# Optimization experiments

Hardware: AMD Instinct MI355X
Metric: run time of the kernel (lower is better)

## Reference

```python
import jax, jax.numpy as jnp
import numpy as np

D_MODEL = 1024
N_HEADS = 16
HEAD_DIM = D_MODEL // N_HEADS
SEQ_LEN = 2048
LN_EPS = 1e-5


def setup_inputs() -> dict:
    key = jax.random.key(0)
    ks = jax.random.split(key, 7)
    s = 1.0 / np.sqrt(D_MODEL)
    h = jax.random.normal(ks[0], (SEQ_LEN, D_MODEL), dtype=jnp.float32)
    # torch nn.Linear weights are (out_features, in_features)
    W_qkv = jax.random.uniform(ks[1], (3 * D_MODEL, D_MODEL), jnp.float32, -s, s)
    b_qkv = jax.random.uniform(ks[2], (3 * D_MODEL,), jnp.float32, -s, s)
    W_out = jax.random.uniform(ks[3], (D_MODEL, D_MODEL), jnp.float32, -s, s)
    b_out = jax.random.uniform(ks[4], (D_MODEL,), jnp.float32, -s, s)
    gamma = jnp.ones((D_MODEL,), jnp.float32)
    beta = jnp.zeros((D_MODEL,), jnp.float32)
    return {"h": h, "W_qkv": W_qkv, "b_qkv": b_qkv, "W_out": W_out,
            "b_out": b_out, "gamma": gamma, "beta": beta}


def reference(h, W_qkv, b_qkv, W_out, b_out, gamma, beta):
    S = h.shape[0]
    # QKV projection: (S, 3*D)
    qkv = h @ W_qkv.T + b_qkv
    q, k, v = jnp.split(qkv, 3, axis=-1)
    # (S, D) -> (H, S, Dh)
    q = q.reshape(S, N_HEADS, HEAD_DIM).transpose(1, 0, 2)
    k = k.reshape(S, N_HEADS, HEAD_DIM).transpose(1, 0, 2)
    v = v.reshape(S, N_HEADS, HEAD_DIM).transpose(1, 0, 2)
    # scaled dot-product attention, non-causal (matches F.sdpa defaults)
    scale = 1.0 / jnp.sqrt(jnp.asarray(HEAD_DIM, dtype=h.dtype))
    scores = jnp.einsum('hqd,hkd->hqk', q, k) * scale  # (H, S, S)
    attn = jax.nn.softmax(scores, axis=-1)
    attn_out = jnp.einsum('hqk,hkd->hqd', attn, v)     # (H, S, Dh)
    attn_out = attn_out.transpose(1, 0, 2).reshape(S, D_MODEL)
    # output projection + residual + LayerNorm
    attn_out = attn_out @ W_out.T + b_out
    x = h + attn_out
    mu = jnp.mean(x, axis=-1, keepdims=True)
    var = jnp.var(x, axis=-1, keepdims=True)
    x_norm = (x - mu) * jax.lax.rsqrt(var + LN_EPS)
    return x_norm * gamma + beta
```

## Files before the change

### kernel.cpp

```cpp
#include <hip/hip_runtime.h>
#include <stdint.h>

#define SEQ 2048
#define DM 1024
#define NH 16
#define DH 64
#define LN_EPS 1e-5f

typedef __bf16 bf16x8 __attribute__((ext_vector_type(8)));
typedef float f32x4 __attribute__((ext_vector_type(4)));
typedef unsigned short u16;
typedef unsigned short u16x8 __attribute__((ext_vector_type(8)));
typedef unsigned int u32;
typedef short s16x4 __attribute__((ext_vector_type(4)));

__device__ __forceinline__ u16 f2bf(float f) {
  unsigned int u = __float_as_uint(f);
  unsigned int r = (u + 0x7fffu + ((u >> 16) & 1u)) >> 16;
  return (u16)r;
}

__device__ __forceinline__ float bf2f(u16 x) {
  return __uint_as_float(((u32)x) << 16);
}

__device__ __forceinline__ u32 packbf(float a, float b) {
  union { __bf16 h[2]; u32 u; } pw;
  pw.h[0] = (__bf16)a; pw.h[1] = (__bf16)b;
  return pw.u;
}

__device__ __forceinline__ f32x4 mfma16x16x16bf(s16x4 a, s16x4 b, f32x4 c) {
#if __has_builtin(__builtin_amdgcn_mfma_f32_16x16x16bf16_1k)
  return __builtin_amdgcn_mfma_f32_16x16x16bf16_1k(a, b, c, 0, 0, 0);
#else
  asm("v_mfma_f32_16x16x16_bf16 %0, %1, %2, %0" : "+v"(c) : "v"(a), "v"(b));
  return c;
#endif
}

#define GLD_LDS16(gp, lp) __builtin_amdgcn_global_load_lds( \
  (const __attribute__((address_space(1))) void*)(gp),      \
  (__attribute__((address_space(3))) void*)(lp), 16, 0, 0)

__global__ __launch_bounds__(256)
void k_f2bf3(const float* __restrict__ a, u16* __restrict__ oa, int na,
             const float* __restrict__ b, u16* __restrict__ ob, int nb,
             const float* __restrict__ c, u16* __restrict__ oc, int nc) {
  int i = blockIdx.x * 256 + threadIdx.x;
  const float* src;
  u16* dst;
  if (i < na) { src = a; dst = oa; }
  else if (i < na + nb) { src = b; dst = ob; i -= na; }
  else if (i < na + nb + nc) { src = c; dst = oc; i -= na + nb; }
  else return;
  float4 v = reinterpret_cast<const float4*>(src)[i];
  ushort4 o;
  o.x = f2bf(v.x); o.y = f2bf(v.y); o.z = f2bf(v.z); o.w = f2bf(v.w);
  reinterpret_cast<ushort4*>(dst)[i] = o;
}

template <int EPI, int BM, int BN, int XCDW>
__global__ __launch_bounds__(256)
void k_gemm_bt(const u16* __restrict__ A, const u16* __restrict__ B,
               const float* __restrict__ bias,
               u16* __restrict__ outb, u16* __restrict__ outv,
               int M, int N, int K) {
  constexpr int MF = BM / 32, NF = BN / 32;
  constexpr int WM = BM / 2, WN = BN / 2;
  constexpr int AG = BM / 64, BG = BN / 64;
  __shared__ u16 Alds[2][BM][32];
  __shared__ u16 Blds[2][BN][32];
  const int tid = threadIdx.x;
  const int w = tid >> 6, l = tid & 63, lg = l >> 4, lr = l & 15;
  const int wr = w >> 1, wc = w & 1;

  int bx = blockIdx.x, by = blockIdx.y, bz = blockIdx.z;
  if (XCDW > 0) {
    const int nx = gridDim.x, ny = gridDim.y;
    const int u = bx + nx * (by + ny * bz);
    const int xcd = u & 7, g = u >> 3;
    bx = xcd * XCDW + (g % XCDW);
    const int rem = g / XCDW;
    by = rem % ny;
    bz = rem / ny;
  }

  const int m0 = by * BM, n0 = bx * BN;
  const int KTall = K >> 5;
  const int ktn = KTall / gridDim.z;
  const int kt0 = bz * ktn;

  f32x4 acc[MF][NF] = {};

  auto stage = [&](int buf, int kt) {
    const int k0 = kt << 5;
    const int row = l >> 2, col = (l & 3) * 8;
#pragma unroll
    for (int p = 0; p < AG; ++p) {
      const int rbase = (w * AG + p) * 16;
      GLD_LDS16(A + (size_t)(m0 + rbase + row) * K + k0 + col, &Alds[buf][rbase][0]);
    }
#pragma unroll
    for (int p = 0; p < BG; ++p) {
      const int rbase = (w * BG + p) * 16;
      GLD_LDS16(B + (size_t)(n0 + rbase + row) * K + k0 + col, &Blds[buf][rbase][0]);
    }
  };

  auto compute = [&](int buf) {
    bf16x8 af[MF], bfr[NF];
#pragma unroll
    for (int mi = 0; mi < MF; ++mi)
      af[mi] = *reinterpret_cast<const bf16x8*>(&Alds[buf][wr * WM + mi * 16 + lr][lg * 8]);
#pragma unroll
    for (int ni = 0; ni < NF; ++ni)
      bfr[ni] = *reinterpret_cast<const bf16x8*>(&Blds[buf][wc * WN + ni * 16 + lr][lg * 8]);
#pragma unroll
    for (int mi = 0; mi < MF; ++mi)
#pragma unroll
      for (int ni = 0; ni < NF; ++ni)
        acc[mi][ni] = __builtin_amdgcn_mfma_f32_16x16x32_bf16(af[mi], bfr[ni], acc[mi][ni], 0, 0, 0);
  };

  stage(0, kt0);
  __syncthreads();
  for (int i = 0; i < ktn; ++i) {
    const int cur = i & 1;
    if (i + 1 < ktn) stage(cur ^ 1, kt0 + i + 1);
    compute(cur);
    __syncthreads();
  }

  if (EPI == 3) {
    u16* op = outb + (size_t)bz * M * N;
#pragma unroll
    for (int ni = 0; ni < NF; ++ni) {
      const int n = n0 + wc * WN + ni * 16 + lr;
#pragma unroll
      for (int mi = 0; mi < MF; ++mi) {
#pragma unroll
        for (int r = 0; r < 4; ++r) {
          const int m = m0 + wr * WM + mi * 16 + lg * 4 + r;
          op[(size_t)m * N + n] = f2bf(acc[mi][ni][r]);
        }
      }
    }
  } else {
    if (n0 < 2048) {
#pragma unroll
      for (int ni = 0; ni < NF; ++ni) {
        const int n = n0 + wc * WN + ni * 16 + lr;
        const float bn = bias[n];
#pragma unroll
        for (int mi = 0; mi < MF; ++mi) {
#pragma unroll
          for (int r = 0; r < 4; ++r) {
            const int m = m0 + wr * WM + mi * 16 + lg * 4 + r;
            outb[(size_t)m * 2048 + n] = f2bf(acc[mi][ni][r] + bn);
          }
        }
      }
    } else {
#pragma unroll
      for (int ni = 0; ni < NF; ++ni) {
        const int n = n0 + wc * WN + ni * 16 + lr;
        const float bn = bias[n];
#pragma unroll
        for (int mi = 0; mi < MF; ++mi) {
          const int mb = m0 + wr * WM + mi * 16 + lg * 4;
          ushort4 pk;
          pk.x = f2bf(acc[mi][ni][0] + bn);
          pk.y = f2bf(acc[mi][ni][1] + bn);
          pk.z = f2bf(acc[mi][ni][2] + bn);
          pk.w = f2bf(acc[mi][ni][3] + bn);
          *reinterpret_cast<ushort4*>(&outv[(size_t)(n - 2048) * M + mb]) = pk;
        }
      }
    }
  }
}

template <int KSPLIT>
__global__ __launch_bounds__(256)
void k_attn(const u16* __restrict__ qk, const u16* __restrict__ vt,
            u16* __restrict__ Opart, float* __restrict__ lsum_out) {
  __shared__ u16 Klds[2][64 * 64];
  __shared__ u16 Vlds[2][64 * 64];
  const int tid = threadIdx.x;
  const int w = tid >> 6, l = tid & 63, lg = l >> 4, lr = l & 15;

  const int u = blockIdx.x + 16 * (blockIdx.y + NH * blockIdx.z);
  const int xcd = u & 7, g = u >> 3;
  const int h = 2 * xcd + (g / (16 * KSPLIT));
  const int rem = g % (16 * KSPLIT);
  const int sp = rem >> 4;
  const int qb2 = rem & 15;

  constexpr int NT = (SEQ / 64) / KSPLIT;
  const int kb0 = sp * NT;

  bf16x8 qfA[2], qfB[2];
  {
    const size_t qrowA = (size_t)(qb2 * 128 + w * 16 + lr) * 2048 + h * 64;
    qfA[0] = *reinterpret_cast<const bf16x8*>(&qk[qrowA + lg * 8]);
    qfA[1] = *reinterpret_cast<const bf16x8*>(&qk[qrowA + 32 + lg * 8]);
    const size_t qrowB = qrowA + (size_t)64 * 2048;
    qfB[0] = *reinterpret_cast<const bf16x8*>(&qk[qrowB + lg * 8]);
    qfB[1] = *reinterpret_cast<const bf16x8*>(&qk[qrowB + 32 + lg * 8]);
  }

  const int sr0 = w * 16 + (l >> 3);
  const int sc0 = ((l & 7) ^ (sr0 & 7)) * 8;
  const int sr1 = sr0 + 8;
  const int sc1 = ((l & 7) ^ (sr1 & 7)) * 8;
  const u16* kb_base = qk + 1024 + h * 64;
  const u16* vb_base = vt + (size_t)(h * 64) * 2048;

  auto stage = [&](int buf, int kb) {
    const u16* k0 = kb_base + (size_t)(kb * 64 + sr0) * 2048 + sc0;
    const u16* k1 = kb_base + (size_t)(kb * 64 + sr1) * 2048 + sc1;
    const u16* v0 = vb_base + (size_t)sr0 * 2048 + kb * 64 + sc0;
    const u16* v1 = vb_base + (size_t)sr1 * 2048 + kb * 64 + sc1;
    GLD_LDS16(k0, &Klds[buf][(w * 16) * 64]);
    GLD_LDS16(k1, &Klds[buf][(w * 16 + 8) * 64]);
    GLD_LDS16(v0, &Vlds[buf][(w * 16) * 64]);
    GLD_LDS16(v1, &Vlds[buf][(w * 16 + 8) * 64]);
  };

  auto kread = [&](int buf, int row, int kbyte) -> bf16x8 {
    const int off = row * 128 + (kbyte ^ ((row & 7) << 4));
    return *reinterpret_cast<const bf16x8*>(
        reinterpret_cast<const char*>(&Klds[buf][0]) + off);
  };

  f32x4 oaccA[4] = {}, oaccB[4] = {};
  f32x4 laccA = {}, laccB = {};
  const float SC = 0.18033688011112042f;
  const s16x4 ONES = {(short)0x3F80, (short)0x3F80, (short)0x3F80, (short)0x3F80};

  stage(0, kb0);
  __syncthreads();

  for (int t = 0; t < NT; ++t) {
    const int cur = t & 1;
    if (t + 1 < NT) stage(cur ^ 1, kb0 + t + 1);

    u32 pawA[4][2], pawB[4][2];
    __builtin_amdgcn_s_setprio(1);
#pragma unroll
    for (int nt = 0; nt < 4; ++nt) {
      bf16x8 kf0 = kread(cur, nt * 16 + lr, lg * 16);
      bf16x8 kf1 = kread(cur, nt * 16 + lr, 64 + lg * 16);
      f32x4 aA = {}, aB = {};
      aA = __builtin_amdgcn_mfma_f32_16x16x32_bf16(kf0, qfA[0], aA, 0, 0, 0);
      aA = __builtin_amdgcn_mfma_f32_16x16x32_bf16(kf1, qfA[1], aA, 0, 0, 0);
      aB = __builtin_amdgcn_mfma_f32_16x16x32_bf16(kf0, qfB[0], aB, 0, 0, 0);
      aB = __builtin_amdgcn_mfma_f32_16x16x32_bf16(kf1, qfB[1], aB, 0, 0, 0);
      float pA[4], pB[4];
#pragma unroll
      for (int r = 0; r < 4; ++r) {
        pA[r] = exp2f(fmaf(aA[r], SC, -8.0f));
        pB[r] = exp2f(fmaf(aB[r], SC, -8.0f));
      }
      pawA[nt][0] = packbf(pA[0], pA[1]);
      pawA[nt][1] = packbf(pA[2], pA[3]);
      pawB[nt][0] = packbf(pB[0], pB[1]);
      pawB[nt][1] = packbf(pB[2], pB[3]);
    }

#pragma unroll
    for (int nt = 0; nt < 4; ++nt) {
      union { u32 wd[2]; s16x4 v; } paA, paB;
      paA.wd[0] = pawA[nt][0]; paA.wd[1] = pawA[nt][1];
      paB.wd[0] = pawB[nt][0]; paB.wd[1] = pawB[nt][1];
      laccA = mfma16x16x16bf(paA.v, ONES, laccA);
      laccB = mfma16x16x16bf(paB.v, ONES, laccB);
#pragma unroll
      for (int nd = 0; nd < 4; ++nd) {
        const int row = nd * 16 + lr;
        const int off = row * 128 + ((nt * 32 + lg * 8) ^ ((row & 7) << 4));
        s16x4 vf = *reinterpret_cast<const s16x4*>(
            reinterpret_cast<const char*>(&Vlds[cur][0]) + off);
        oaccA[nd] = mfma16x16x16bf(paA.v, vf, oaccA[nd]);
        oaccB[nd] = mfma16x16x16bf(paB.v, vf, oaccB[nd]);
      }
    }
    __builtin_amdgcn_s_setprio(0);
    __syncthreads();
  }

  const size_t obase = (size_t)sp * SEQ * DM;
#pragma unroll
  for (int r = 0; r < 4; ++r) {
    const size_t qA = qb2 * 128 + w * 16 + lg * 4 + r;
    const size_t rowA = obase + qA * DM + h * 64;
    const size_t rowB = rowA + (size_t)64 * DM;
#pragma unroll
    for (int nd = 0; nd < 4; ++nd) {
      Opart[rowA + nd * 16 + lr] = f2bf(oaccA[nd][r]);
      Opart[rowB + nd * 16 + lr] = f2bf(oaccB[nd][r]);
    }
  }
  if (lr == 0) {
    const size_t lbase = ((size_t)sp * NH + h) * SEQ + qb2 * 128 + w * 16;
#pragma unroll
    for (int r = 0; r < 4; ++r) {
      lsum_out[lbase + lg * 4 + r] = laccA[r];
      lsum_out[lbase + 64 + lg * 4 + r] = laccB[r];
    }
  }
}

template <int KSPLIT>
__global__ __launch_bounds__(256)
void k_combine(const u16* __restrict__ Opart, const float* __restrict__ lsum,
               u16* __restrict__ attn_out) {
  const int row = blockIdx.x, tid = threadIdx.x;
  const int h = tid >> 4;
  float den = 0.f;
#pragma unroll
  for (int s = 0; s < KSPLIT; ++s)
    den += lsum[((size_t)s * NH + h) * SEQ + row];
  const float inv = 1.f / den;
  float o[4] = {0.f, 0.f, 0.f, 0.f};
#pragma unroll
  for (int s = 0; s < KSPLIT; ++s) {
    const ushort4 v = reinterpret_cast<const ushort4*>(
        Opart + ((size_t)s * SEQ + row) * DM)[tid];
    o[0] += bf2f(v.x); o[1] += bf2f(v.y);
    o[2] += bf2f(v.z); o[3] += bf2f(v.w);
  }
  ushort4 pk;
  pk.x = f2bf(o[0] * inv); pk.y = f2bf(o[1] * inv);
  pk.z = f2bf(o[2] * inv); pk.w = f2bf(o[3] * inv);
  reinterpret_cast<ushort4*>(attn_out + (size_t)row * DM)[tid] = pk;
}

__global__ __launch_bounds__(256)
void k_ln(const float* __restrict__ hin, const u16* __restrict__ pp,
          const float* __restrict__ bout, const float* __restrict__ gamma,
          const float* __restrict__ beta, float* __restrict__ out) {
  const int row = blockIdx.x, tid = threadIdx.x;
  const float4 hv = reinterpret_cast<const float4*>(hin + (size_t)row * DM)[tid];
  const ushort4 p0 = reinterpret_cast<const ushort4*>(pp + (size_t)row * DM)[tid];
  const ushort4 p1 = reinterpret_cast<const ushort4*>(pp + (size_t)(SEQ + row) * DM)[tid];
  const float4 bv = reinterpret_cast<const float4*>(bout)[tid];
  float4 v;
  v.x = hv.x + bf2f(p0.x) + bf2f(p1.x) + bv.x;
  v.y = hv.y + bf2f(p0.y) + bf2f(p1.y) + bv.y;
  v.z = hv.z + bf2f(p0.z) + bf2f(p1.z) + bv.z;
  v.w = hv.w + bf2f(p0.w) + bf2f(p1.w) + bv.w;
  float s = v.x + v.y + v.z + v.w;
  float q = v.x * v.x + v.y * v.y + v.z * v.z + v.w * v.w;
#pragma unroll
  for (int m = 1; m < 64; m <<= 1) { s += __shfl_xor(s, m); q += __shfl_xor(q, m); }
  __shared__ float sh[8];
  const int w = tid >> 6;
  if ((tid & 63) == 0) { sh[w] = s; sh[4 + w] = q; }
  __syncthreads();
  s = sh[0] + sh[1] + sh[2] + sh[3];
  q = sh[4] + sh[5] + sh[6] + sh[7];
  const float mu = s * (1.f / 1024.f);
  const float var = q * (1.f / 1024.f) - mu * mu;
  const float rstd = rsqrtf(var + LN_EPS);
  float4 g = reinterpret_cast<const float4*>(gamma)[tid];
  float4 b = reinterpret_cast<const float4*>(beta)[tid];
  float4 o;
  o.x = (v.x - mu) * rstd * g.x + b.x;
  o.y = (v.y - mu) * rstd * g.y + b.y;
  o.z = (v.z - mu) * rstd * g.z + b.z;
  o.w = (v.w - mu) * rstd * g.w + b.w;
  reinterpret_cast<float4*>(out + (size_t)row * DM)[tid] = o;
}

extern "C" void kernel_launch(void* const* d_in, const int* in_sizes, int n_in,
                              void* d_out, int out_size, void* d_ws, size_t ws_size,
                              hipStream_t stream) {
  const float* h     = (const float*)d_in[0];
  const float* Wqkv  = (const float*)d_in[1];
  const float* bqkv  = (const float*)d_in[2];
  const float* Wout  = (const float*)d_in[3];
  const float* bout  = (const float*)d_in[4];
  const float* gamma = (const float*)d_in[5];
  const float* beta  = (const float*)d_in[6];
  float* out = (float*)d_out;

  char* ws = (char*)d_ws;
  u16* h_bf      = (u16*)(ws);
  u16* Wqkv_bf   = (u16*)(ws + (size_t)4 * 1024 * 1024);
  u16* Wout_bf   = (u16*)(ws + (size_t)10 * 1024 * 1024);
  u16* qk_bf     = (u16*)(ws + (size_t)12 * 1024 * 1024);
  u16* vt_bf     = (u16*)(ws + (size_t)20 * 1024 * 1024);
  u16* attn_bf   = (u16*)(ws + (size_t)24 * 1024 * 1024);
  u16* Opart     = (u16*)(ws + (size_t)28 * 1024 * 1024);
  u16* Opp       = (u16*)(ws + (size_t)44 * 1024 * 1024);
  float* lsums   = (float*)(ws + (size_t)52 * 1024 * 1024);

  const int na = SEQ * DM / 4, nb = 3 * DM * DM / 4, nc = DM * DM / 4;
  k_f2bf3<<<(na + nb + nc + 255) / 256, 256, 0, stream>>>(
      h, h_bf, na, Wqkv, Wqkv_bf, nb, Wout, Wout_bf, nc);

  k_gemm_bt<2, 64, 128, 3><<<dim3(24, 32), 256, 0, stream>>>(
      h_bf, Wqkv_bf, bqkv, qk_bf, vt_bf, SEQ, 3 * DM, DM);

  k_attn<4><<<dim3(16, 16, 4), 256, 0, stream>>>(qk_bf, vt_bf, Opart, lsums);
  k_combine<4><<<SEQ, 256, 0, stream>>>(Opart, lsums, attn_bf);

  k_gemm_bt<3, 64, 64, 2><<<dim3(16, 32, 2), 256, 0, stream>>>(
      attn_bf, Wout_bf, nullptr, Opp, nullptr, SEQ, DM, DM);

  k_ln<<<SEQ, 256, 0, stream>>>(h, Opp, bout, gamma, beta, out);
}
```

Measured before the change: 94.46 us.

## Double GEMM K-tile to 64 with XOR-swizzled LDS layout

New measurement: 85.92 us. -9.0%, faster.

```diff
diff --git a/kernel.cpp b/kernel.cpp
--- a/kernel.cpp
+++ b/kernel.cpp
@@ -68,9 +68,8 @@
                int M, int N, int K) {
   constexpr int MF = BM / 32, NF = BN / 32;
   constexpr int WM = BM / 2, WN = BN / 2;
-  constexpr int AG = BM / 64, BG = BN / 64;
-  __shared__ u16 Alds[2][BM][32];
-  __shared__ u16 Blds[2][BN][32];
+  __shared__ u16 Alds[2][BM][64];
+  __shared__ u16 Blds[2][BN][64];
   const int tid = threadIdx.x;
   const int w = tid >> 6, l = tid & 63, lg = l >> 4, lr = l & 15;
   const int wr = w >> 1, wc = w & 1;
@@ -87,40 +86,55 @@
   }
 
   const int m0 = by * BM, n0 = bx * BN;
-  const int KTall = K >> 5;
+  const int KTall = K >> 6;
   const int ktn = KTall / gridDim.z;
   const int kt0 = bz * ktn;
 
   f32x4 acc[MF][NF] = {};
 
+  const int srow = l >> 3;
+  const int scol = ((l & 7) ^ (srow & 7)) * 8;
   auto stage = [&](int buf, int kt) {
-    const int k0 = kt << 5;
-    const int row = l >> 2, col = (l & 3) * 8;
-#pragma unroll
-    for (int p = 0; p < AG; ++p) {
-      const int rbase = (w * AG + p) * 16;
-      GLD_LDS16(A + (size_t)(m0 + rbase + row) * K + k0 + col, &Alds[buf][rbase][0]);
-    }
-#pragma unroll
-    for (int p = 0; p < BG; ++p) {
-      const int rbase = (w * BG + p) * 16;
-      GLD_LDS16(B + (size_t)(n0 + rbase + row) * K + k0 + col, &Blds[buf][rbase][0]);
-    }
+    const int k0 = kt << 6;
+#pragma unroll
+    for (int p = 0; p < BM / 32; ++p) {
+      const int rbase = (w * (BM / 32) + p) * 8;
+      GLD_LDS16(A + (size_t)(m0 + rbase + srow) * K + k0 + scol, &Alds[buf][rbase][0]);
+    }
+#pragma unroll
+    for (int p = 0; p < BN / 32; ++p) {
+      const int rbase = (w * (BN / 32) + p) * 8;
+      GLD_LDS16(B + (size_t)(n0 + rbase + srow) * K + k0 + scol, &Blds[buf][rbase][0]);
+    }
+  };
+
+  auto aread = [&](int buf, int row, int kbyte) -> bf16x8 {
+    const int off = row * 128 + (kbyte ^ ((row & 7) << 4));
+    return *reinterpret_cast<const bf16x8*>(
+        reinterpret_cast<const char*>(&Alds[buf][0][0]) + off);
+  };
+  auto bread = [&](int buf, int row, int kbyte) -> bf16x8 {
+    const int off = row * 128 + (kbyte ^ ((row & 7) << 4));
+    return *reinterpret_cast<const bf16x8*>(
+        reinterpret_cast<const char*>(&Blds[buf][0][0]) + off);
   };
 
   auto compute = [&](int buf) {
-    bf16x8 af[MF], bfr[NF];
-#pragma unroll
-    for (int mi = 0; mi < MF; ++mi)
-      af[mi] = *reinterpret_cast<const bf16x8*>(&Alds[buf][wr * WM + mi * 16 + lr][lg * 8]);
-#pragma unroll
-    for (int ni = 0; ni < NF; ++ni)
-      bfr[ni] = *reinterpret_cast<const bf16x8*>(&Blds[buf][wc * WN + ni * 16 + lr][lg * 8]);
-#pragma unroll
-    for (int mi = 0; mi < MF; ++mi)
+#pragma unroll
+    for (int kk = 0; kk < 2; ++kk) {
+      bf16x8 af[MF], bfr[NF];
+#pragma unroll
+      for (int mi = 0; mi < MF; ++mi)
+        af[mi] = aread(buf, wr * WM + mi * 16 + lr, kk * 64 + lg * 16);
 #pragma unroll
       for (int ni = 0; ni < NF; ++ni)
-        acc[mi][ni] = __builtin_amdgcn_mfma_f32_16x16x32_bf16(af[mi], bfr[ni], acc[mi][ni], 0, 0, 0);
+        bfr[ni] = bread(buf, wc * WN + ni * 16 + lr, kk * 64 + lg * 16);
+#pragma unroll
+      for (int mi = 0; mi < MF; ++mi)
+#pragma unroll
+        for (int ni = 0; ni < NF; ++ni)
+          acc[mi][ni] = __builtin_amdgcn_mfma_f32_16x16x32_bf16(af[mi], bfr[ni], acc[mi][ni], 0, 0, 0);
+    }
   };
 
   stage(0, kt0);
```
